# Kernel optimization log

Measured on AMD Instinct MI355X. Metric: run time of the kernel, lower is better.

Reference implementation:

```python
import jax, jax.numpy as jnp
import numpy as np

V = 32000; D = 1024; L = 2; H = 16; KVH = 4; HD = D // H; E = 8; FF = 2048; K = 2
B = 2; S = 1024; WINDOW = 4096; THETA = 10000.0; EPS = 1e-6


def setup_inputs() -> dict:
    key = jax.random.key(0)
    ks = jax.random.split(key, 12)
    std = 0.02
    return {
        'tokens': jax.random.randint(ks[0], (B, S), 0, V),
        'tok_emb': jax.random.normal(ks[1], (V, D), jnp.float32),  # nn.Embedding default N(0,1)
        'norm1_w': jnp.ones((L, D), jnp.float32),
        'norm2_w': jnp.ones((L, D), jnp.float32),
        'wq': jax.random.normal(ks[2], (L, D, D), jnp.float32) * std,
        'wk': jax.random.normal(ks[3], (L, KVH * HD, D), jnp.float32) * std,
        'wv': jax.random.normal(ks[4], (L, KVH * HD, D), jnp.float32) * std,
        'wo': jax.random.normal(ks[5], (L, D, D), jnp.float32) * std,
        'router_w': jax.random.normal(ks[6], (L, E, D), jnp.float32) * (std / np.sqrt(D)),
        'w1': jax.random.normal(ks[7], (L, E, FF, D), jnp.float32) * std,
        'w2': jax.random.normal(ks[8], (L, E, FF, D), jnp.float32) * std,
        'w3': jax.random.normal(ks[9], (L, E, D, FF), jnp.float32) * std,
        'normf_w': jnp.ones((D,), jnp.float32),
        'head_w': jax.random.normal(ks[10], (V, D), jnp.float32) * std,
    }


def rmsnorm(x, w):
    # F.normalize(x, dim=-1, eps) * w * sqrt(d)
    n = jnp.linalg.norm(x, axis=-1, keepdims=True)
    return x / jnp.maximum(n, EPS) * w * np.float32(np.sqrt(x.shape[-1]))


def rope(x, cos, sin):
    # x: (b, s, h, hd); pairs are interleaved (even, odd) per view_as_complex
    x2 = x.reshape(x.shape[:-1] + (-1, 2))
    x0, x1 = x2[..., 0], x2[..., 1]
    o0 = x0 * cos - x1 * sin
    o1 = x0 * sin + x1 * cos
    return jnp.stack([o0, o1], axis=-1).reshape(x.shape)


def attention(x, wq, wk, wv, wo, cos, sin):
    b, s, _ = x.shape
    q = (x @ wq.T).reshape(b, s, H, HD)
    k = (x @ wk.T).reshape(b, s, KVH, HD)
    v = (x @ wv.T).reshape(b, s, KVH, HD)
    q = rope(q, cos, sin)
    k = rope(k, cos, sin)
    g = H // KVH
    k = jnp.repeat(k, g, axis=2)
    v = jnp.repeat(v, g, axis=2)
    scores = jnp.einsum('bqhd,bkhd->bhqk', q, k) / np.float32(np.sqrt(HD))
    i = jnp.arange(s)[:, None]; j = jnp.arange(s)[None, :]
    allow = (j <= i) & (i - j < WINDOW)  # causal + sliding window
    scores = jnp.where(allow, scores, -jnp.inf)
    attn = jax.nn.softmax(scores, axis=-1)
    out = jnp.einsum('bhqk,bkhd->bqhd', attn, v).reshape(b, s, D)
    return out @ wo.T


def moe(x, router_w, w1, w2, w3):
    b, s, d = x.shape
    logits = jnp.einsum('bsd,ed->bse', x, router_w)
    probs = jax.nn.softmax(logits, axis=-1)
    _, idx = jax.lax.top_k(probs, K)                      # (b, s, K)
    mask = jax.nn.one_hot(idx, E, dtype=x.dtype).sum(-2)  # (b, s, E) binary
    xt = x.reshape(-1, d)           # (T, d)
    mt = mask.reshape(-1, E)        # (T, E)
    # Dense masked dispatch: every expert computed on all tokens, combine masks to zero
    u = jnp.einsum('td,efd->etf', xt, w1)
    g = jax.nn.silu(u) * jnp.einsum('td,efd->etf', xt, w2)
    y = jnp.einsum('etf,edf->etd', g, w3)
    out = jnp.einsum('etd,te->td', y, mt).reshape(b, s, d)  # unweighted combine (per source)
    # aux losses
    z_loss = jnp.mean(jax.scipy.special.logsumexp(logits, axis=-1)) ** 2
    load = probs.sum(axis=0)  # (s, E), matching probs.sum(dim=0) in source
    load_loss = (jnp.std(load, ddof=1) / jnp.mean(load)) ** 2
    aux = 0.001 * z_loss + 0.001 * load_loss
    return out, aux


def _rope_tables(dtype):
    freqs = 1.0 / (THETA ** (np.arange(0, HD, 2, dtype=np.float32) / HD))
    ang = np.arange(S, dtype=np.float32)[:, None] * freqs[None, :]
    cos = jnp.asarray(np.cos(ang), dtype)[None, :, None, :]
    sin = jnp.asarray(np.sin(ang), dtype)[None, :, None, :]
    return cos, sin


def reference(tokens, tok_emb, norm1_w, norm2_w, wq, wk, wv, wo, router_w, w1, w2, w3, normf_w, head_w):
    x = tok_emb[tokens]  # (B, S, D)
    cos, sin = _rope_tables(x.dtype)
    attn_scale = np.float32(1.0 / np.sqrt(2.0 * L))
    aux_total = jnp.zeros((), x.dtype)
    for l in range(L):
        x = x + attn_scale * attention(rmsnorm(x, norm1_w[l]), wq[l], wk[l], wv[l], wo[l], cos, sin)
        mo, aux = moe(rmsnorm(x, norm2_w[l]), router_w[l], w1[l], w2[l], w3[l])
        x = x + mo
        aux_total = aux_total + aux
    logits = rmsnorm(x, normf_w) @ head_w.T
    return logits, aux_total
```

## Files before the change

### kernel.cpp

```cpp
#include <hip/hip_runtime.h>
#include <math.h>

#define DEV __device__ __forceinline__

using v8s = __attribute__((ext_vector_type(8))) short;
using v4f = __attribute__((ext_vector_type(4))) float;

DEV short f2bf(float f) {
    unsigned u = __float_as_uint(f);
    unsigned r = (u + 0x7fffu + ((u >> 16) & 1u)) >> 16;
    return (short)(unsigned short)r;
}
DEV float bf2f(short s) {
    return __uint_as_float(((unsigned)(unsigned short)s) << 16);
}

DEV void gload16(const short* g, short* l) {
    __builtin_amdgcn_global_load_lds((const __attribute__((address_space(1))) void*)g,
                                     (__attribute__((address_space(3))) void*)l,
                                     16, 0, 0);
}

DEV float block_sum256(float v, float* red) {
    __syncthreads();
#pragma unroll
    for (int o = 32; o >= 1; o >>= 1) v += __shfl_down(v, o, 64);
    if ((threadIdx.x & 63) == 0) red[threadIdx.x >> 6] = v;
    __syncthreads();
    return red[0] + red[1] + red[2] + red[3];
}
DEV float block_max256(float v, float* red) {
    __syncthreads();
#pragma unroll
    for (int o = 32; o >= 1; o >>= 1) v = fmaxf(v, __shfl_down(v, o, 64));
    if ((threadIdx.x & 63) == 0) red[threadIdx.x >> 6] = v;
    __syncthreads();
    return fmaxf(fmaxf(red[0], red[1]), fmaxf(red[2], red[3]));
}

DEV long tile_goff(int row, int g) {
    return ((long)(g >> 2) << 12) + ((long)(g & 3) << 10) + ((long)(row & 127) << 3);
}


__global__ __launch_bounds__(256) void conv_tile(const float* __restrict__ src,
                                                 short* __restrict__ hi, short* __restrict__ lo,
                                                 long nGroups, int Kg, long chunkRows, long chunkPanelStride) {
    const long panelElems = 128L * Kg * 8;
    for (long idx = (long)blockIdx.x * 256 + threadIdx.x; idx < nGroups; idx += (long)gridDim.x * 256) {
        long rrow = idx / Kg; int g = (int)(idx - rrow * Kg);
        long c = rrow / chunkRows; int ri = (int)(rrow - c * chunkRows);
        long panel = c * chunkPanelStride + (ri >> 7);
        long dst = panel * panelElems + ((long)(g >> 2) << 12) + ((long)(g & 3) << 10) + ((long)(ri & 127) << 3);
        const float4 f0 = ((const float4*)src)[idx * 2];
        const float4 f1 = ((const float4*)src)[idx * 2 + 1];
        short h0 = f2bf(f0.x), h1 = f2bf(f0.y), h2 = f2bf(f0.z), h3 = f2bf(f0.w);
        short h4 = f2bf(f1.x), h5 = f2bf(f1.y), h6 = f2bf(f1.z), h7 = f2bf(f1.w);
        *(ushort4*)(hi + dst)     = make_ushort4((unsigned short)h0, (unsigned short)h1,
                                                 (unsigned short)h2, (unsigned short)h3);
        *(ushort4*)(hi + dst + 4) = make_ushort4((unsigned short)h4, (unsigned short)h5,
                                                 (unsigned short)h6, (unsigned short)h7);
        if (lo) {
            short l0 = f2bf(f0.x - bf2f(h0)), l1 = f2bf(f0.y - bf2f(h1));
            short l2 = f2bf(f0.z - bf2f(h2)), l3 = f2bf(f0.w - bf2f(h3));
            short l4 = f2bf(f1.x - bf2f(h4)), l5 = f2bf(f1.y - bf2f(h5));
            short l6 = f2bf(f1.z - bf2f(h6)), l7 = f2bf(f1.w - bf2f(h7));
            *(ushort4*)(lo + dst)     = make_ushort4((unsigned short)l0, (unsigned short)l1,
                                                     (unsigned short)l2, (unsigned short)l3);
            *(ushort4*)(lo + dst + 4) = make_ushort4((unsigned short)l4, (unsigned short)l5,
                                                     (unsigned short)l6, (unsigned short)l7);
        }
    }
}

struct GemmP {
    const short* Ah; const short* Al;
    const short* Bh; const short* Bl;
    float* C; short* Ch; short* Cl;
    const int* cnt; const int* ppd; const int* lrow;
    long aPanelsZ;
    long strideAz;
    long strideBz, strideCz;
    int M, N, K, lda, ldc;
    float alpha;
    int outMode;
    int gqaB;
    int grouped;
    int causalSkip;
    int causalK;
    int ntiles, S, G;
};

template<bool SPLIT, bool AREG>
__global__ __launch_bounds__(256) void gemm_bt(GemmP p) {
    const int lid = blockIdx.x;
    const int xcd = lid & 7, sI = lid >> 3;
    const int gi = xcd + 8 * (sI / p.S);
    if (gi >= p.G) return;
    const int mt = sI % p.S;
    const int nt = gi % p.ntiles;
    const int z  = gi / p.ntiles;
    if (p.causalSkip && nt > mt) return;

    const int tid = threadIdx.x;

    int Mz = p.grouped ? p.cnt[z] : p.M;
    if (mt * 128 >= Mz) return;

    long bOff;
    if (p.gqaB) { int b = z >> 4, h = z & 15; bOff = (long)(b * 4 + (h >> 2)) * p.strideBz; }
    else bOff = (long)z * p.strideBz;

    extern __shared__ char smem[];
    short* Ahs = (short*)smem;
    short* Bhs = Ahs + 4096;
    short* Als = Bhs + 4096;
    short* Bls = Als + 4096;

    const int lane = tid & 63, w = tid >> 6;
    const int lr = lane & 15, lg = lane >> 4;
    const int wr = w >> 1, wc = w & 1;

    v4f acc[4][4];
#pragma unroll
    for (int i = 0; i < 4; ++i)
#pragma unroll
        for (int j = 0; j < 4; ++j) { acc[i][j][0] = 0.f; acc[i][j][1] = 0.f; acc[i][j][2] = 0.f; acc[i][j][3] = 0.f; }

    const short* bks  = p.Bh + bOff + (long)nt * 128 * p.K + (long)w * 1024 + lane * 8;
    const short* bksL = SPLIT ? p.Bl + bOff + (long)nt * 128 * p.K + (long)w * 1024 + lane * 8 : nullptr;
    short* dB  = Bhs + w * 1024;
    short* dBl = Bls + w * 1024;

    const short *aks = nullptr, *aksL = nullptr;
    short *dA = nullptr, *dAl = nullptr;
    const short *aH = nullptr, *aL = nullptr;
    short *sA0 = nullptr, *sA1 = nullptr, *sA0l = nullptr, *sA1l = nullptr;
    if constexpr (AREG) {
        const int r = tid & 127;
        const int kgA = tid >> 7;
        int am = mt * 128 + r; if (am >= Mz) am = Mz - 1;
        long arowoff = (long)z * p.strideAz + (long)am * p.lda;
        aH = p.Ah + arowoff + kgA * 16;
        aL = SPLIT ? p.Al + arowoff + kgA * 16 : nullptr;
        sA0 = Ahs + (kgA * 256 + r) * 8; sA1 = sA0 + 1024;
        sA0l = Als + (kgA * 256 + r) * 8; sA1l = sA0l + 1024;
    } else {
        long aPanel = (p.grouped ? (long)(p.ppd[z] >> 7) : (long)z * p.aPanelsZ) + mt;
        aks  = p.Ah + aPanel * 128L * p.K + (long)w * 1024 + lane * 8;
        aksL = SPLIT ? p.Al + aPanel * 128L * p.K + (long)w * 1024 + lane * 8 : nullptr;
        dA  = Ahs + w * 1024;
        dAl = Als + w * 1024;
    }

    const int kEnd = p.causalK ? min(p.K, (mt + 1) * 128) : p.K;

    for (int k0 = 0; k0 < kEnd; k0 += 32) {
        const long kb = (long)k0 * 128;
        uint4 a0, a1, a0l, a1l;
        if constexpr (AREG) {
            a0 = *(const uint4*)(aH + k0);
            a1 = *(const uint4*)(aH + k0 + 8);
            if (SPLIT) { a0l = *(const uint4*)(aL + k0); a1l = *(const uint4*)(aL + k0 + 8); }
        }
        __syncthreads();
        gload16(bks + kb,       dB);
        gload16(bks + kb + 512, dB + 512);
        if (SPLIT) {
            gload16(bksL + kb,       dBl);
            gload16(bksL + kb + 512, dBl + 512);
        }
        if constexpr (AREG) {
            *(uint4*)sA0 = a0; *(uint4*)sA1 = a1;
            if (SPLIT) { *(uint4*)sA0l = a0l; *(uint4*)sA1l = a1l; }
        } else {
            gload16(aks + kb,       dA);
            gload16(aks + kb + 512, dA + 512);
            if (SPLIT) {
                gload16(aksL + kb,       dAl);
                gload16(aksL + kb + 512, dAl + 512);
            }
        }
        __syncthreads();
        const int abase = lg * 1024 + (wr * 64 + lr) * 8;
        const int bbase = lg * 1024 + (wc * 64 + lr) * 8;
        v8s ah[4], bh[4];
#pragma unroll
        for (int i = 0; i < 4; ++i) {
            ah[i] = *(const v8s*)(Ahs + abase + i * 128);
            bh[i] = *(const v8s*)(Bhs + bbase + i * 128);
        }
        if constexpr (SPLIT) {
            v8s al[4], bl[4];
#pragma unroll
            for (int i = 0; i < 4; ++i) {
                al[i] = *(const v8s*)(Als + abase + i * 128);
                bl[i] = *(const v8s*)(Bls + bbase + i * 128);
            }
#pragma unroll
            for (int mi = 0; mi < 4; ++mi)
#pragma unroll
                for (int nj = 0; nj < 4; ++nj) {
                    acc[mi][nj] = __builtin_amdgcn_mfma_f32_16x16x32_bf16(ah[mi], bh[nj], acc[mi][nj], 0, 0, 0);
                    acc[mi][nj] = __builtin_amdgcn_mfma_f32_16x16x32_bf16(al[mi], bh[nj], acc[mi][nj], 0, 0, 0);
                    acc[mi][nj] = __builtin_amdgcn_mfma_f32_16x16x32_bf16(ah[mi], bl[nj], acc[mi][nj], 0, 0, 0);
                }
        } else {
#pragma unroll
            for (int mi = 0; mi < 4; ++mi)
#pragma unroll
                for (int nj = 0; nj < 4; ++nj)
                    acc[mi][nj] = __builtin_amdgcn_mfma_f32_16x16x32_bf16(ah[mi], bh[nj], acc[mi][nj], 0, 0, 0);
        }
    }

#pragma unroll
    for (int mi = 0; mi < 4; ++mi) {
        const int mrow = mt * 128 + wr * 64 + mi * 16 + lg * 4;
#pragma unroll
        for (int nj = 0; nj < 4; ++nj) {
            const int ncol = nt * 128 + wc * 64 + nj * 16 + lr;
            if (ncol < p.N) {
#pragma unroll
                for (int rr = 0; rr < 4; ++rr) {
                    const int m = mrow + rr;
                    if (m < Mz) {
                        float v = acc[mi][nj][rr] * p.alpha;
                        if (p.outMode == 3) {
                            int b = z >> 4, h = z & 15;
                            int grow = b * 1024 + m, col = h * 64 + ncol;
                            long dst = ((long)(grow >> 7)) * 131072 + ((long)(col >> 5) << 12)
                                     + ((long)((col >> 3) & 3) << 10) + ((long)(grow & 127) << 3) + (col & 7);
                            short hi = f2bf(v);
                            p.Ch[dst] = hi;
                            p.Cl[dst] = f2bf(v - bf2f(hi));
                        } else {
                            long crow;
                            if (p.grouped == 1)      crow = p.ppd[z] + m;
                            else if (p.grouped == 2) crow = p.lrow[z * 2048 + m];
                            else                     crow = m;
                            long co = (long)z * p.strideCz + crow * (long)p.ldc + ncol;
                            if (p.outMode == 0) p.C[co] = v;
                            else                p.C[co] += v;
                        }
                    }
                }
            }
        }
    }
}

__global__ __launch_bounds__(256) void embed_kernel(const int* toks, const float* emb, float* X) {
    const int t = blockIdx.x;
    const int tok = toks[t];
    const float4* s = (const float4*)(emb + (size_t)tok * 1024);
    float4* d = (float4*)(X + (size_t)t * 1024);
    d[threadIdx.x] = s[threadIdx.x];
}

__global__ __launch_bounds__(256) void rmsnorm_split(const float* X, const float* w, short* oh, short* ol) {
    __shared__ float red[4];
    const long t = blockIdx.x;
    const float* r = X + t * 1024;
    float ss = 0.f;
    for (int j = threadIdx.x; j < 1024; j += 256) { float f = r[j]; ss += f * f; }
    ss = block_sum256(ss, red);
    const float sc = 32.f / fmaxf(sqrtf(ss), 1e-6f);
    if (threadIdx.x < 128) {
        const int g = threadIdx.x, f = g * 8;
        float v[8];
#pragma unroll
        for (int j = 0; j < 8; ++j) v[j] = r[f + j] * sc * w[f + j];
        long dst = (t >> 7) * 131072 + ((long)(g >> 2) << 12) + ((long)(g & 3) << 10) + ((t & 127) << 3);
        short h[8], lo[8];
#pragma unroll
        for (int j = 0; j < 8; ++j) { h[j] = f2bf(v[j]); lo[j] = f2bf(v[j] - bf2f(h[j])); }
        *(ushort4*)(oh + dst)     = make_ushort4((unsigned short)h[0], (unsigned short)h[1], (unsigned short)h[2], (unsigned short)h[3]);
        *(ushort4*)(oh + dst + 4) = make_ushort4((unsigned short)h[4], (unsigned short)h[5], (unsigned short)h[6], (unsigned short)h[7]);
        *(ushort4*)(ol + dst)     = make_ushort4((unsigned short)lo[0], (unsigned short)lo[1], (unsigned short)lo[2], (unsigned short)lo[3]);
        *(ushort4*)(ol + dst + 4) = make_ushort4((unsigned short)lo[4], (unsigned short)lo[5], (unsigned short)lo[6], (unsigned short)lo[7]);
    }
}

struct RopeF { float f[32]; };

__global__ __launch_bounds__(256) void rope_q_kernel(const float* QKV, short* OH, short* OL, RopeF rf) {
    const int idx = blockIdx.x * 256 + threadIdx.x;
    const int pp = idx & 31, h = (idx >> 5) & 15, s = (idx >> 9) & 1023, b = idx >> 19;
    const float* src = QKV + ((size_t)(b * 1024 + s)) * 1536 + h * 64 + 2 * pp;
    const float x0 = src[0], x1 = src[1];
    const float ang = (float)s * rf.f[pp];
    float sn, cs; sincosf(ang, &sn, &cs);
    const float o0 = x0 * cs - x1 * sn, o1 = x0 * sn + x1 * cs;
    const int z = b * 16 + h, d = 2 * pp;
    const long off = (long)z * 65536 + (long)(s >> 7) * 8192
                   + ((long)(d >> 5) << 12) + ((long)((d >> 3) & 3) << 10)
                   + ((long)(s & 127) << 3) + (d & 7);
    short h0 = f2bf(o0); OH[off] = h0; OL[off] = f2bf(o0 - bf2f(h0));
    short h1 = f2bf(o1); OH[off + 1] = h1; OL[off + 1] = f2bf(o1 - bf2f(h1));
}

__global__ __launch_bounds__(256) void rope_k_kernel(const float* QKV, short* KH, short* KL, RopeF rf) {
    const int idx = blockIdx.x * 256 + threadIdx.x;
    const int pp = idx & 31, kv = (idx >> 5) & 3, s = (idx >> 7) & 1023, b = idx >> 17;
    const float* src = QKV + ((size_t)(b * 1024 + s)) * 1536 + 1024 + kv * 64 + 2 * pp;
    const float x0 = src[0], x1 = src[1];
    const float ang = (float)s * rf.f[pp];
    float sn, cs; sincosf(ang, &sn, &cs);
    const float o0 = x0 * cs - x1 * sn, o1 = x0 * sn + x1 * cs;
    const int z = b * 4 + kv, d = 2 * pp;
    const long off = (long)z * 65536 + (long)(s >> 7) * 8192
                   + ((long)(d >> 5) << 12) + ((long)((d >> 3) & 3) << 10)
                   + ((long)(s & 127) << 3) + (d & 7);
    short h0 = f2bf(o0); KH[off] = h0; KL[off] = f2bf(o0 - bf2f(h0));
    short h1 = f2bf(o1); KH[off + 1] = h1; KL[off + 1] = f2bf(o1 - bf2f(h1));
}

__global__ __launch_bounds__(256) void transpose_v_kernel(const float* QKV, short* VH, short* VL) {
    const int idx = blockIdx.x * 256 + threadIdx.x;
    const int d = idx & 63, kv = (idx >> 6) & 3, s = (idx >> 8) & 1023, b = idx >> 18;
    const float f = QKV[((size_t)(b * 1024 + s)) * 1536 + 1280 + kv * 64 + d];
    const int z = b * 4 + kv;
    const long off = (long)z * 131072 + ((long)(s >> 5) << 12) + ((long)((s >> 3) & 3) << 10)
                   + ((long)d << 3) + (s & 7);
    short hi = f2bf(f);
    VH[off] = hi; VL[off] = f2bf(f - bf2f(hi));
    VH[off + 512] = 0; VL[off + 512] = 0;
}

__global__ __launch_bounds__(256) void attn_softmax(float* SC) {
    const long row = blockIdx.x;
    const int i = (int)(row & 1023);
    float* r = SC + row * 1024;
    __shared__ float buf[1024];
    __shared__ float red[4];
    const int n = i + 1;
    for (int j = threadIdx.x; j < 1024; j += 256) buf[j] = r[j];
    __syncthreads();
    float m = -INFINITY;
    for (int j = threadIdx.x; j < n; j += 256) m = fmaxf(m, buf[j]);
    m = block_max256(m, red);
    float s = 0.f;
    for (int j = threadIdx.x; j < n; j += 256) { float e = expf(buf[j] - m); buf[j] = e; s += e; }
    s = block_sum256(s, red);
    const float inv = 1.f / s;
    short* rh = (short*)r;
    short* rl = rh + 1024;
    __syncthreads();
    for (int j = threadIdx.x; j < 1024; j += 256) {
        float pv = (j < n) ? buf[j] * inv : 0.f;
        short hi = f2bf(pv);
        rh[j] = hi;
        rl[j] = f2bf(pv - bf2f(hi));
    }
}

__global__ __launch_bounds__(256) void router_kernel(const float* X, const float* wn, const float* rw,
                                                     float* probs, float* lse, int* cnt, int* ltok, int* lrow) {
    __shared__ float xs[1024];
    __shared__ float red[4];
    __shared__ float lg[8];
    const int t = blockIdx.x;
    const float* r = X + (size_t)t * 1024;
    for (int j = threadIdx.x; j < 1024; j += 256) xs[j] = r[j];
    __syncthreads();
    float ss = 0.f;
    for (int j = threadIdx.x; j < 1024; j += 256) ss += xs[j] * xs[j];
    ss = block_sum256(ss, red);
    const float sc = 32.f / fmaxf(sqrtf(ss), 1e-6f);
    float acc[8] = {0, 0, 0, 0, 0, 0, 0, 0};
    for (int j = threadIdx.x; j < 1024; j += 256) {
        const float xv = xs[j] * wn[j];
#pragma unroll
        for (int e = 0; e < 8; ++e) acc[e] += xv * rw[e * 1024 + j];
    }
#pragma unroll
    for (int e = 0; e < 8; ++e) {
        float s = block_sum256(acc[e], red);
        if (threadIdx.x == 0) lg[e] = s * sc;
    }
    __syncthreads();
    if (threadIdx.x == 0) {
        float m = lg[0];
        for (int e = 1; e < 8; ++e) m = fmaxf(m, lg[e]);
        float ex[8], se = 0.f;
        for (int e = 0; e < 8; ++e) { ex[e] = expf(lg[e] - m); se += ex[e]; }
        const float inv = 1.f / se;
        float pr[8];
        for (int e = 0; e < 8; ++e) { pr[e] = ex[e] * inv; probs[(size_t)t * 8 + e] = pr[e]; }
        lse[t] = m + logf(se);
        int i1 = 0;
        for (int e = 1; e < 8; ++e) if (pr[e] > pr[i1]) i1 = e;
        int i2 = (i1 == 0) ? 1 : 0;
        for (int e = 0; e < 8; ++e) if (e != i1 && pr[e] > pr[i2]) i2 = e;
        int s1 = atomicAdd(&cnt[i1], 1); ltok[i1 * 2048 + s1] = t; lrow[i1 * 2048 + s1] = 2 * t;
        int s2 = atomicAdd(&cnt[i2], 1); ltok[i2 * 2048 + s2] = t; lrow[i2 * 2048 + s2] = 2 * t + 1;
    }
}

__global__ void prefix_kernel(const int* cnt, int* ppd) {
    if (threadIdx.x == 0 && blockIdx.x == 0) {
        int a = 0;
        for (int e = 0; e < 8; ++e) { ppd[e] = a; a += ((cnt[e] + 127) >> 7) << 7; }
    }
}

__global__ __launch_bounds__(256) void gather_kernel(const short* XNH, const short* XNL,
                                                     const int* cnt, const int* ppd, const int* ltok,
                                                     short* GXNH, short* GXNL) {
    const int e = blockIdx.y, i = blockIdx.x;
    if (i >= cnt[e]) return;
    const int t = ltok[e * 2048 + i];
    const int pd = ppd[e] + i;
    const int plane = threadIdx.x >> 7, g = threadIdx.x & 127;
    const long goff = ((long)(g >> 2) << 12) + ((long)(g & 3) << 10);
    const long src = (long)(t >> 7) * 131072 + goff + ((t & 127) << 3);
    const long dst = (long)(pd >> 7) * 131072 + goff + ((pd & 127) << 3);
    const short* S = plane ? XNL : XNH;
    short* D = plane ? GXNL : GXNH;
    *(uint4*)(D + dst) = *(const uint4*)(S + src);
}

__global__ __launch_bounds__(256) void silu_mul(const float* U, short* HH, short* HL) {
    const int row = blockIdx.x, g = threadIdx.x;
    const float* ur = U + (long)row * 4096 + g * 8;
    const float4 u0 = *(const float4*)ur, u1 = *(const float4*)(ur + 4);
    const float4 g0 = *(const float4*)(ur + 2048), g1 = *(const float4*)(ur + 2052);
    float h[8];
    h[0] = (u0.x / (1.f + expf(-u0.x))) * g0.x;
    h[1] = (u0.y / (1.f + expf(-u0.y))) * g0.y;
    h[2] = (u0.z / (1.f + expf(-u0.z))) * g0.z;
    h[3] = (u0.w / (1.f + expf(-u0.w))) * g0.w;
    h[4] = (u1.x / (1.f + expf(-u1.x))) * g1.x;
    h[5] = (u1.y / (1.f + expf(-u1.y))) * g1.y;
    h[6] = (u1.z / (1.f + expf(-u1.z))) * g1.z;
    h[7] = (u1.w / (1.f + expf(-u1.w))) * g1.w;
    const long dst = (long)(row >> 7) * 262144 + ((long)(g >> 2) << 12) + ((long)(g & 3) << 10) + ((row & 127) << 3);
    short hh[8], ll[8];
#pragma unroll
    for (int j = 0; j < 8; ++j) { hh[j] = f2bf(h[j]); ll[j] = f2bf(h[j] - bf2f(hh[j])); }
    *(ushort4*)(HH + dst)     = make_ushort4((unsigned short)hh[0], (unsigned short)hh[1], (unsigned short)hh[2], (unsigned short)hh[3]);
    *(ushort4*)(HH + dst + 4) = make_ushort4((unsigned short)hh[4], (unsigned short)hh[5], (unsigned short)hh[6], (unsigned short)hh[7]);
    *(ushort4*)(HL + dst)     = make_ushort4((unsigned short)ll[0], (unsigned short)ll[1], (unsigned short)ll[2], (unsigned short)ll[3]);
    *(ushort4*)(HL + dst + 4) = make_ushort4((unsigned short)ll[4], (unsigned short)ll[5], (unsigned short)ll[6], (unsigned short)ll[7]);
}

__global__ __launch_bounds__(256) void combine_kernel(float* X, const float* Y) {
    const int i4 = blockIdx.x * 256 + threadIdx.x;
    const int t = i4 >> 8, d4 = i4 & 255;
    float4 x = ((float4*)X)[i4];
    const float4 a = ((const float4*)Y)[(size_t)(2 * t) * 256 + d4];
    const float4 b = ((const float4*)Y)[(size_t)(2 * t + 1) * 256 + d4];
    x.x += a.x + b.x; x.y += a.y + b.y; x.z += a.z + b.z; x.w += a.w + b.w;
    ((float4*)X)[i4] = x;
}

__global__ __launch_bounds__(256) void aux_kernel(const float* probs, const float* lse, float* auxb, int layer) {
    __shared__ float red[4];
    float sl = 0.f;
    for (int t = threadIdx.x; t < 2048; t += 256) sl += lse[t];
    sl = block_sum256(sl, red);
    float s1 = 0.f, s2 = 0.f;
    for (int i = threadIdx.x; i < 8192; i += 256) {
        const float l = probs[i] + probs[8192 + i];
        s1 += l; s2 += l * l;
    }
    s1 = block_sum256(s1, red);
    s2 = block_sum256(s2, red);
    if (threadIdx.x == 0) {
        const float ml = sl / 2048.f;
        const float mean = s1 / 8192.f;
        const float var = fmaxf((s2 - s1 * s1 / 8192.f) / 8191.f, 0.f);
        auxb[layer] = 0.001f * (ml * ml + var / (mean * mean));
    }
}

__global__ void finalize_aux(const float* auxb, float* out) {
    if (threadIdx.x == 0 && blockIdx.x == 0)
        out[(size_t)2 * 1024 * 32000] = auxb[0] + auxb[1];
}

static void run_gemm(hipStream_t s, bool split, bool areg, GemmP& p, int ntiles, int mtiles, int zdim) {
    p.ntiles = ntiles; p.S = mtiles;
    p.G = ntiles * zdim;
    int Gp = (p.G + 7) & ~7;
    long nb = (long)Gp * mtiles;
    dim3 g((unsigned)nb, 1, 1), b(256);
    if (split) {
        if (areg) gemm_bt<true, true><<<g, b, 32768, s>>>(p);
        else      gemm_bt<true, false><<<g, b, 32768, s>>>(p);
    } else {
        if (areg) gemm_bt<false, true><<<g, b, 16384, s>>>(p);
        else      gemm_bt<false, false><<<g, b, 16384, s>>>(p);
    }
}

static void run_tile(hipStream_t s, const float* src, short* hi, short* lo,
                     long rows, int K, long chunkRows, long chunkPanelStride) {
    long groups = rows * (K / 8);
    long nb = (groups + 255) / 256; if (nb > 2048) nb = 2048;
    conv_tile<<<(unsigned)nb, 256, 0, s>>>(src, hi, lo, groups, K / 8, chunkRows, chunkPanelStride);
}

extern "C" void kernel_launch(void* const* d_in, const int* in_sizes, int n_in,
                              void* d_out, int out_size, void* d_ws, size_t ws_size,
                              hipStream_t stream) {
    (void)in_sizes; (void)n_in; (void)out_size; (void)ws_size;
    const int*   tokens = (const int*)d_in[0];
    const float* tok_emb = (const float*)d_in[1];
    const float* norm1 = (const float*)d_in[2];
    const float* norm2 = (const float*)d_in[3];
    const float* wq = (const float*)d_in[4];
    const float* wk = (const float*)d_in[5];
    const float* wv = (const float*)d_in[6];
    const float* wo = (const float*)d_in[7];
    const float* rw = (const float*)d_in[8];
    const float* w1 = (const float*)d_in[9];
    const float* w2 = (const float*)d_in[10];
    const float* w3 = (const float*)d_in[11];
    const float* normf = (const float*)d_in[12];
    const float* headw = (const float*)d_in[13];
    float* out = (float*)d_out;

    char* w = (char*)d_ws;
    const size_t MB = 1024ull * 1024ull;
    float* X    = (float*)(w + 0);
    short* XNH  = (short*)(w + 8 * MB);
    short* XNL  = (short*)(w + 12 * MB);
    short* QRH  = (short*)(w + 16 * MB);
    short* QRL  = (short*)(w + 20 * MB);
    short* AOH  = QRH;
    short* AOL  = QRL;
    short* KRH  = (short*)(w + 24 * MB);
    short* KRL  = (short*)(w + 25 * MB);
    short* VTH  = (short*)(w + 26 * MB);
    short* VTL  = (short*)(w + 28 * MB);
    float* QKV  = (float*)(w + 32 * MB);
    float* SC   = (float*)(w + 32 * MB);
    float* U    = (float*)(w + 32 * MB);
    short* HH   = (short*)(w + 112 * MB);
    short* HL   = (short*)(w + 132 * MB);
    float* Y    = (float*)(w + 152 * MB);
    short* GXNH = (short*)(w + 168 * MB);
    short* GXNL = (short*)(w + 178 * MB);
    float* PROBS= (float*)(w + 188 * MB);
    float* LSE  = (float*)(w + 188 * MB + 65536);
    int*   CNT  = (int*)  (w + 188 * MB + 73728);
    int*   PPD  = (int*)  (w + 188 * MB + 73856);
    int*   LTOK = (int*)  (w + 188 * MB + 74240);
    int*   LROW = (int*)  (w + 188 * MB + 74240 + 65536);
    float* AUXB = (float*)(w + 188 * MB + 74240 + 131072);
    short* WQKVH = (short*)(w + 190 * MB);
    short* WQKVL = (short*)(w + 196 * MB);
    short* WOH   = (short*)(w + 202 * MB);
    short* WOL   = (short*)(w + 206 * MB);
    short* W12H  = (short*)(w + 210 * MB);
    short* W12L  = (short*)(w + 274 * MB);
    short* W3H   = (short*)(w + 338 * MB);
    short* W3L   = (short*)(w + 370 * MB);
    short* HDH   = (short*)(w + 274 * MB);

    RopeF rf;
    for (int i = 0; i < 32; ++i) {
        float t = (float)pow(10000.0, (double)(2 * i) / 64.0);
        rf.f[i] = 1.0f / t;
    }

    for (int l = 0; l < 2; ++l) {
        long qo = (long)l * 1572864;
        run_tile(stream, wq + (long)l * 1048576, WQKVH + qo,           WQKVL + qo,           1024, 1024, 1024, 8);
        run_tile(stream, wk + (long)l * 262144,  WQKVH + qo + 1048576, WQKVL + qo + 1048576, 256, 1024, 256, 2);
        run_tile(stream, wv + (long)l * 262144,  WQKVH + qo + 1310720, WQKVL + qo + 1310720, 256, 1024, 256, 2);
    }
    run_tile(stream, wo, WOH, WOL, 2048, 1024, 2048, 16);

    embed_kernel<<<2048, 256, 0, stream>>>(tokens, tok_emb, X);

    for (int l = 0; l < 2; ++l) {
        const bool msp = (l == 0);
        run_tile(stream, w1 + (long)l * 16777216, W12H,           msp ? W12L : nullptr,           16384, 1024, 2048, 32);
        run_tile(stream, w2 + (long)l * 16777216, W12H + 2097152, msp ? W12L + 2097152 : nullptr, 16384, 1024, 2048, 32);
        run_tile(stream, w3 + (long)l * 16777216, W3H,            msp ? W3L : nullptr,            8192, 2048, 8192, 64);

        rmsnorm_split<<<2048, 256, 0, stream>>>(X, norm1 + l * 1024, XNH, XNL);

        { GemmP p = {}; p.Ah = XNH; p.Al = XNL; p.Bh = WQKVH + (long)l * 1572864; p.Bl = WQKVL + (long)l * 1572864;
          p.C = QKV; p.M = 2048; p.N = 1536; p.K = 1024; p.aPanelsZ = 16; p.ldc = 1536; p.alpha = 1.f;
          run_gemm(stream, true, false, p, 12, 16, 1); }

        rope_q_kernel<<<4096, 256, 0, stream>>>(QKV, QRH, QRL, rf);
        rope_k_kernel<<<1024, 256, 0, stream>>>(QKV, KRH, KRL, rf);
        transpose_v_kernel<<<2048, 256, 0, stream>>>(QKV, VTH, VTL);

        { GemmP p = {}; p.Ah = QRH; p.Al = QRL; p.Bh = KRH; p.Bl = KRL; p.C = SC;
          p.M = 1024; p.N = 1024; p.K = 64; p.aPanelsZ = 8; p.ldc = 1024;
          p.strideBz = 65536; p.strideCz = 1048576;
          p.alpha = 0.125f; p.gqaB = 1; p.causalSkip = 1;
          run_gemm(stream, true, false, p, 8, 8, 32); }

        attn_softmax<<<32768, 256, 0, stream>>>(SC);

        { GemmP p = {}; p.Ah = (short*)SC; p.Al = (short*)SC + 1024; p.Bh = VTH; p.Bl = VTL; p.Ch = AOH; p.Cl = AOL;
          p.M = 1024; p.N = 64; p.K = 1024; p.lda = 2048;
          p.strideAz = 2097152; p.strideBz = 131072;
          p.alpha = 1.f; p.gqaB = 1; p.causalK = 1; p.outMode = 3;
          run_gemm(stream, true, true, p, 1, 8, 32); }

        { GemmP p = {}; p.Ah = AOH; p.Al = AOL; p.Bh = WOH + (long)l * 1048576; p.Bl = WOL + (long)l * 1048576; p.C = X;
          p.M = 2048; p.N = 1024; p.K = 1024; p.aPanelsZ = 16; p.ldc = 1024;
          p.alpha = 0.5f; p.outMode = 1;
          run_gemm(stream, true, false, p, 8, 16, 1); }

        rmsnorm_split<<<2048, 256, 0, stream>>>(X, norm2 + l * 1024, XNH, XNL);
        hipMemsetAsync(CNT, 0, 8 * sizeof(int), stream);
        router_kernel<<<2048, 256, 0, stream>>>(X, norm2 + l * 1024, rw + (size_t)l * 8 * 1024,
                                                PROBS, LSE, CNT, LTOK, LROW);
        prefix_kernel<<<1, 64, 0, stream>>>(CNT, PPD);
        { dim3 gg(2048, 8); gather_kernel<<<gg, 256, 0, stream>>>(XNH, XNL, CNT, PPD, LTOK, GXNH, GXNL); }

        { GemmP p = {}; p.Ah = GXNH; p.Al = GXNL; p.Bh = W12H; p.Bl = W12L; p.C = U;
          p.M = 2048; p.N = 4096; p.K = 1024; p.ldc = 4096;
          p.strideBz = 4194304; p.strideCz = 0; p.alpha = 1.f; p.grouped = 1;
          p.cnt = CNT; p.ppd = PPD; p.lrow = LROW;
          run_gemm(stream, msp, false, p, 32, 16, 8); }
        silu_mul<<<5120, 256, 0, stream>>>(U, HH, HL);
        { GemmP p = {}; p.Ah = HH; p.Al = HL; p.Bh = W3H; p.Bl = W3L; p.C = Y;
          p.M = 2048; p.N = 1024; p.K = 2048; p.ldc = 1024;
          p.strideBz = 2097152; p.strideCz = 0; p.alpha = 1.f; p.grouped = 2;
          p.cnt = CNT; p.ppd = PPD; p.lrow = LROW;
          run_gemm(stream, msp, false, p, 8, 16, 8); }
        combine_kernel<<<2048, 256, 0, stream>>>(X, Y);
        aux_kernel<<<1, 256, 0, stream>>>(PROBS, LSE, AUXB, l);

        if (l == 0)
            run_tile(stream, headw, HDH, nullptr, 32000, 1024, 32000, 250);
    }

    rmsnorm_split<<<2048, 256, 0, stream>>>(X, normf, XNH, XNL);
    { GemmP p = {}; p.Ah = XNH; p.Bh = HDH; p.C = out;
      p.M = 2048; p.N = 32000; p.K = 1024; p.aPanelsZ = 16; p.ldc = 32000; p.alpha = 1.f;
      run_gemm(stream, false, false, p, 250, 16, 1); }
    finalize_aux<<<1, 1, 0, stream>>>(AUXB, out);
}
```

Measured before the change: 2.375 ms.

## Double-buffer LDS tiles in panel-layout GEMM path with async prefetch

For the non-AREG GEMM variant, LDS is split into two buffers so the next K-slice is loaded with global_load_lds while the current slice runs through MFMA. Explicit s_waitcnt vmcnt and raw s_barrier replace the two __syncthreads per iteration. This is meant to hide global-load latency behind compute. In exchange, LDS per block doubles (up to 64KB for the split path), which can lower occupancy.

```diff
diff --git a/kernel.cpp b/kernel.cpp
--- a/kernel.cpp
+++ b/kernel.cpp
@@ -21,6 +21,8 @@
                                      16, 0, 0);
 }
 
+DEV void raw_barrier() { asm volatile("s_barrier" ::: "memory"); }
+
 DEV float block_sum256(float v, float* red) {
     __syncthreads();
 #pragma unroll
@@ -36,10 +38,6 @@
     if ((threadIdx.x & 63) == 0) red[threadIdx.x >> 6] = v;
     __syncthreads();
     return fmaxf(fmaxf(red[0], red[1]), fmaxf(red[2], red[3]));
-}
-
-DEV long tile_goff(int row, int g) {
-    return ((long)(g >> 2) << 12) + ((long)(g & 3) << 10) + ((long)(row & 127) << 3);
 }
 
 
@@ -112,10 +110,8 @@
     else bOff = (long)z * p.strideBz;
 
     extern __shared__ char smem[];
-    short* Ahs = (short*)smem;
-    short* Bhs = Ahs + 4096;
-    short* Als = Bhs + 4096;
-    short* Bls = Als + 4096;
+    short* s0 = (short*)smem;
+    const int BUF = SPLIT ? 16384 : 8192;
 
     const int lane = tid & 63, w = tid >> 6;
     const int lr = lane & 15, lg = lane >> 4;
@@ -129,11 +125,8 @@
 
     const short* bks  = p.Bh + bOff + (long)nt * 128 * p.K + (long)w * 1024 + lane * 8;
     const short* bksL = SPLIT ? p.Bl + bOff + (long)nt * 128 * p.K + (long)w * 1024 + lane * 8 : nullptr;
-    short* dB  = Bhs + w * 1024;
-    short* dBl = Bls + w * 1024;
 
     const short *aks = nullptr, *aksL = nullptr;
-    short *dA = nullptr, *dAl = nullptr;
     const short *aH = nullptr, *aL = nullptr;
     short *sA0 = nullptr, *sA1 = nullptr, *sA0l = nullptr, *sA1l = nullptr;
     if constexpr (AREG) {
@@ -143,74 +136,139 @@
         long arowoff = (long)z * p.strideAz + (long)am * p.lda;
         aH = p.Ah + arowoff + kgA * 16;
         aL = SPLIT ? p.Al + arowoff + kgA * 16 : nullptr;
-        sA0 = Ahs + (kgA * 256 + r) * 8; sA1 = sA0 + 1024;
-        sA0l = Als + (kgA * 256 + r) * 8; sA1l = sA0l + 1024;
+        sA0 = s0 + (kgA * 256 + r) * 8; sA1 = sA0 + 1024;
+        sA0l = s0 + 8192 + (kgA * 256 + r) * 8; sA1l = sA0l + 1024;
     } else {
         long aPanel = (p.grouped ? (long)(p.ppd[z] >> 7) : (long)z * p.aPanelsZ) + mt;
         aks  = p.Ah + aPanel * 128L * p.K + (long)w * 1024 + lane * 8;
         aksL = SPLIT ? p.Al + aPanel * 128L * p.K + (long)w * 1024 + lane * 8 : nullptr;
-        dA  = Ahs + w * 1024;
-        dAl = Als + w * 1024;
     }
 
     const int kEnd = p.causalK ? min(p.K, (mt + 1) * 128) : p.K;
 
-    for (int k0 = 0; k0 < kEnd; k0 += 32) {
-        const long kb = (long)k0 * 128;
-        uint4 a0, a1, a0l, a1l;
-        if constexpr (AREG) {
-            a0 = *(const uint4*)(aH + k0);
-            a1 = *(const uint4*)(aH + k0 + 8);
+    if constexpr (!AREG) {
+        const int nIter = kEnd >> 5;
+        const int wb = w * 1024;
+        {
+            const long kb = 0;
+            short* base = s0;
+            gload16(aks + kb,       base + wb);
+            gload16(aks + kb + 512, base + wb + 512);
+            gload16(bks + kb,       base + 4096 + wb);
+            gload16(bks + kb + 512, base + 4096 + wb + 512);
+            if (SPLIT) {
+                gload16(aksL + kb,       base + 8192 + wb);
+                gload16(aksL + kb + 512, base + 8192 + wb + 512);
+                gload16(bksL + kb,       base + 12288 + wb);
+                gload16(bksL + kb + 512, base + 12288 + wb + 512);
+            }
+        }
+        for (int i = 0; i < nIter; ++i) {
+            const int cur = i & 1;
+            if (i + 1 < nIter) {
+                raw_barrier();
+                const long kb = (long)(i + 1) * 4096;
+                short* base = s0 + (cur ^ 1) * BUF;
+                gload16(aks + kb,       base + wb);
+                gload16(aks + kb + 512, base + wb + 512);
+                gload16(bks + kb,       base + 4096 + wb);
+                gload16(bks + kb + 512, base + 4096 + wb + 512);
+                if (SPLIT) {
+                    gload16(aksL + kb,       base + 8192 + wb);
+                    gload16(aksL + kb + 512, base + 8192 + wb + 512);
+                    gload16(bksL + kb,       base + 12288 + wb);
+                    gload16(bksL + kb + 512, base + 12288 + wb + 512);
+                }
+                if constexpr (SPLIT) asm volatile("s_waitcnt vmcnt(8)" ::: "memory");
+                else                 asm volatile("s_waitcnt vmcnt(4)" ::: "memory");
+            } else {
+                asm volatile("s_waitcnt vmcnt(0)" ::: "memory");
+            }
+            raw_barrier();
+            const short* base = s0 + cur * BUF;
+            const int abase = lg * 1024 + (wr * 64 + lr) * 8;
+            const int bbase = 4096 + lg * 1024 + (wc * 64 + lr) * 8;
+            v8s ah[4], bh[4];
+#pragma unroll
+            for (int q = 0; q < 4; ++q) {
+                ah[q] = *(const v8s*)(base + abase + q * 128);
+                bh[q] = *(const v8s*)(base + bbase + q * 128);
+            }
+            if constexpr (SPLIT) {
+                v8s al[4], bl[4];
+#pragma unroll
+                for (int q = 0; q < 4; ++q) {
+                    al[q] = *(const v8s*)(base + 8192 + abase + q * 128);
+                    bl[q] = *(const v8s*)(base + 8192 + bbase + q * 128);
+                }
+#pragma unroll
+                for (int mi = 0; mi < 4; ++mi)
+#pragma unroll
+                    for (int nj = 0; nj < 4; ++nj) {
+                        acc[mi][nj] = __builtin_amdgcn_mfma_f32_16x16x32_bf16(ah[mi], bh[nj], acc[mi][nj], 0, 0, 0);
+                        acc[mi][nj] = __builtin_amdgcn_mfma_f32_16x16x32_bf16(al[mi], bh[nj], acc[mi][nj], 0, 0, 0);
+                        acc[mi][nj] = __builtin_amdgcn_mfma_f32_16x16x32_bf16(ah[mi], bl[nj], acc[mi][nj], 0, 0, 0);
+                    }
+            } else {
+#pragma unroll
+                for (int mi = 0; mi < 4; ++mi)
+#pragma unroll
+                    for (int nj = 0; nj < 4; ++nj)
+                        acc[mi][nj] = __builtin_amdgcn_mfma_f32_16x16x32_bf16(ah[mi], bh[nj], acc[mi][nj], 0, 0, 0);
+            }
+        }
+    } else {
+        short* Ahs = s0;
+        short* Bhs = s0 + 4096;
+        short* Als = s0 + 8192;
+        short* Bls = s0 + 12288;
+        const int wb = w * 1024;
+        for (int k0 = 0; k0 < kEnd; k0 += 32) {
+            const long kb = (long)k0 * 128;
+            uint4 a0 = *(const uint4*)(aH + k0);
+            uint4 a1 = *(const uint4*)(aH + k0 + 8);
+            uint4 a0l, a1l;
             if (SPLIT) { a0l = *(const uint4*)(aL + k0); a1l = *(const uint4*)(aL + k0 + 8); }
-        }
-        __syncthreads();
-        gload16(bks + kb,       dB);
-        gload16(bks + kb + 512, dB + 512);
-        if (SPLIT) {
-            gload16(bksL + kb,       dBl);
-            gload16(bksL + kb + 512, dBl + 512);
-        }
-        if constexpr (AREG) {
+            __syncthreads();
+            gload16(bks + kb,       Bhs + wb);
+            gload16(bks + kb + 512, Bhs + wb + 512);
+            if (SPLIT) {
+                gload16(bksL + kb,       Bls + wb);
+                gload16(bksL + kb + 512, Bls + wb + 512);
+            }
             *(uint4*)sA0 = a0; *(uint4*)sA1 = a1;
             if (SPLIT) { *(uint4*)sA0l = a0l; *(uint4*)sA1l = a1l; }
-        } else {
-            gload16(aks + kb,       dA);
-            gload16(aks + kb + 512, dA + 512);
-            if (SPLIT) {
-                gload16(aksL + kb,       dAl);
-                gload16(aksL + kb + 512, dAl + 512);
+            __syncthreads();
+            const int abase = lg * 1024 + (wr * 64 + lr) * 8;
+            const int bbase = lg * 1024 + (wc * 64 + lr) * 8;
+            v8s ah[4], bh[4];
+#pragma unroll
+            for (int q = 0; q < 4; ++q) {
+                ah[q] = *(const v8s*)(Ahs + abase + q * 128);
+                bh[q] = *(const v8s*)(Bhs + bbase + q * 128);
             }
-        }
-        __syncthreads();
-        const int abase = lg * 1024 + (wr * 64 + lr) * 8;
-        const int bbase = lg * 1024 + (wc * 64 + lr) * 8;
-        v8s ah[4], bh[4];
-#pragma unroll
-        for (int i = 0; i < 4; ++i) {
-            ah[i] = *(const v8s*)(Ahs + abase + i * 128);
-            bh[i] = *(const v8s*)(Bhs + bbase + i * 128);
-        }
-        if constexpr (SPLIT) {
-            v8s al[4], bl[4];
-#pragma unroll
-            for (int i = 0; i < 4; ++i) {
-                al[i] = *(const v8s*)(Als + abase + i * 128);
-                bl[i] = *(const v8s*)(Bls + bbase + i * 128);
+            if constexpr (SPLIT) {
+                v8s al[4], bl[4];
+#pragma unroll
+                for (int q = 0; q < 4; ++q) {
+                    al[q] = *(const v8s*)(Als + abase + q * 128);
+                    bl[q] = *(const v8s*)(Bls + bbase + q * 128);
+                }
+#pragma unroll
+                for (int mi = 0; mi < 4; ++mi)
+#pragma unroll
+                    for (int nj = 0; nj < 4; ++nj) {
+                        acc[mi][nj] = __builtin_amdgcn_mfma_f32_16x16x32_bf16(ah[mi], bh[nj], acc[mi][nj], 0, 0, 0);
+                        acc[mi][nj] = __builtin_amdgcn_mfma_f32_16x16x32_bf16(al[mi], bh[nj], acc[mi][nj], 0, 0, 0);
+                        acc[mi][nj] = __builtin_amdgcn_mfma_f32_16x16x32_bf16(ah[mi], bl[nj], acc[mi][nj], 0, 0, 0);
+                    }
+            } else {
+#pragma unroll
+                for (int mi = 0; mi < 4; ++mi)
+#pragma unroll
+                    for (int nj = 0; nj < 4; ++nj)
+                        acc[mi][nj] = __builtin_amdgcn_mfma_f32_16x16x32_bf16(ah[mi], bh[nj], acc[mi][nj], 0, 0, 0);
             }
-#pragma unroll
-            for (int mi = 0; mi < 4; ++mi)
-#pragma unroll
-                for (int nj = 0; nj < 4; ++nj) {
-                    acc[mi][nj] = __builtin_amdgcn_mfma_f32_16x16x32_bf16(ah[mi], bh[nj], acc[mi][nj], 0, 0, 0);
-                    acc[mi][nj] = __builtin_amdgcn_mfma_f32_16x16x32_bf16(al[mi], bh[nj], acc[mi][nj], 0, 0, 0);
-                    acc[mi][nj] = __builtin_amdgcn_mfma_f32_16x16x32_bf16(ah[mi], bl[nj], acc[mi][nj], 0, 0, 0);
-                }
-        } else {
-#pragma unroll
-            for (int mi = 0; mi < 4; ++mi)
-#pragma unroll
-                for (int nj = 0; nj < 4; ++nj)
-                    acc[mi][nj] = __builtin_amdgcn_mfma_f32_16x16x32_bf16(ah[mi], bh[nj], acc[mi][nj], 0, 0, 0);
         }
     }
 
@@ -486,12 +544,13 @@
     int Gp = (p.G + 7) & ~7;
     long nb = (long)Gp * mtiles;
     dim3 g((unsigned)nb, 1, 1), b(256);
+    size_t lds = areg ? (split ? 32768 : 16384) : (split ? 65536 : 32768);
     if (split) {
-        if (areg) gemm_bt<true, true><<<g, b, 32768, s>>>(p);
-        else      gemm_bt<true, false><<<g, b, 32768, s>>>(p);
+        if (areg) gemm_bt<true, true><<<g, b, lds, s>>>(p);
+        else      gemm_bt<true, false><<<g, b, lds, s>>>(p);
     } else {
-        if (areg) gemm_bt<false, true><<<g, b, 16384, s>>>(p);
-        else      gemm_bt<false, false><<<g, b, 16384, s>>>(p);
+        if (areg) gemm_bt<false, true><<<g, b, lds, s>>>(p);
+        else      gemm_bt<false, false><<<g, b, lds, s>>>(p);
     }
 }
 
```

New measurement: 2.209 ms. -7.0%, faster.
